# Kernel optimization log

Hardware: AMD Instinct MI355X
Metric: run time of the kernel (lower is better)

## Reference

```python
import jax, jax.numpy as jnp
import numpy as np

N_EMB = 4096
EMB_DIM = 256
BETA = 0.25


def setup_inputs() -> dict:
    key = jax.random.key(0)
    k1, k2 = jax.random.split(key)
    z = jax.random.normal(k1, (32, EMB_DIM, 32, 32), dtype=jnp.float32)
    # nn.Embedding weight initialized uniform(-1/n_emb, 1/n_emb)
    embedding = jax.random.uniform(
        k2, (N_EMB, EMB_DIM), dtype=jnp.float32,
        minval=-1.0 / N_EMB, maxval=1.0 / N_EMB)
    return {"z": z, "embedding": embedding}


def reference(z, embedding):
    sg = jax.lax.stop_gradient
    # (B,C,H,W) -> (B,H,W,C)
    zp = jnp.transpose(z, (0, 2, 3, 1))
    zf = zp.reshape(-1, EMB_DIM)  # [N, D]
    # squared distances: ||z||^2 + ||e||^2 - 2 z e^T  -> [N, n_emb]
    d = (jnp.sum(zf * zf, axis=1, keepdims=True)
         + jnp.sum(embedding * embedding, axis=1)
         - 2.0 * jnp.matmul(zf, embedding.T))
    idx = jnp.argmin(d, axis=1)  # [N]
    min_encodings = jax.nn.one_hot(idx, N_EMB, dtype=zf.dtype)  # [N, n_emb]
    e_mean = jnp.mean(min_encodings, axis=0)
    perplexity = jnp.exp(-jnp.sum(e_mean * jnp.log(e_mean + 1e-10)))
    # gather codebook rows (same math as one-hot matmul)
    z_q = jnp.take(embedding, idx, axis=0).reshape(zp.shape)
    # straight-through estimator
    z_q_st = zp + sg(z_q - zp)
    q_latent_loss = jnp.mean((z_q_st - sg(zp)) ** 2)
    e_latent_loss = jnp.mean((sg(z_q_st) - zp) ** 2)
    loss = q_latent_loss + BETA * e_latent_loss
    z_q_out = jnp.transpose(z_q_st, (0, 3, 1, 2))  # (B,C,H,W)
    return (loss, z_q_out, perplexity, min_encodings, idx[:, None])
```

## Files before the change

### kernel.cpp

```cpp
#include <hip/hip_runtime.h>

#define N_ROWS 32768
#define NEMB   4096
#define DIM    256

#define O_LOSS 0
#define O_ZQ   1ull
#define O_PERP 8388609ull
#define O_ENC  8388610ull
#define O_IDX  142606338ull
#define Z4_BEG 2097153
#define Z4_END 35651584

#define CAP    32
#define EPS    1e-3f

typedef unsigned long long u64;
typedef __attribute__((ext_vector_type(8))) __bf16 bf16x8;
typedef __attribute__((ext_vector_type(4))) float  f32x4;


__device__ __forceinline__ unsigned int f2bf1(float x) {
    unsigned int u = __float_as_uint(x);
    return (u + 0x7fffu + ((u >> 16) & 1u)) >> 16;
}
__device__ __forceinline__ unsigned int f2bf2(float lo, float hi) {
    return f2bf1(lo) | (f2bf1(hi) << 16);
}

__global__ __launch_bounds__(256)
void vq_zero(float* __restrict__ out)
{
    const f32x4 zz = {0.f, 0.f, 0.f, 0.f};
    const size_t base = (size_t)Z4_BEG + (size_t)blockIdx.x * 256 + threadIdx.x;
#pragma unroll
    for (int i = 0; i < 64; ++i) {
        const size_t idx = base + (size_t)i * 524288;
        if (idx < (size_t)Z4_END)
            __builtin_nontemporal_store(zz, (f32x4*)out + idx);
    }
}

__global__ __launch_bounds__(256)
void vq_prep(const float* __restrict__ z, const float* __restrict__ emb,
             unsigned short* __restrict__ zbf, unsigned short* __restrict__ embsw,
             int* __restrict__ counts, float* __restrict__ out)
{
    const int tid = threadIdx.x, blk = blockIdx.x;
    if (blk < 1024) {
        __shared__ float L[32][256];
        const int b = blk >> 5, sub = blk & 31;
        const int c0 = (sub >> 2) << 5;
        const int hw0 = (sub & 3) << 8;
        const float* zp = z + (size_t)b * 262144 + hw0 + tid;
#pragma unroll 8
        for (int i = 0; i < 32; ++i)
            L[i][tid] = zp[(size_t)(c0 + i) << 10];
        __syncthreads();
        const int n = (b << 10) + hw0 + tid;
        unsigned int pk[16];
#pragma unroll
        for (int c2 = 0; c2 < 16; ++c2)
            pk[c2] = f2bf2(L[2 * c2][tid], L[2 * c2 + 1][tid]);
        uint4* dst = (uint4*)((char*)zbf + (size_t)n * 512 + (size_t)c0 * 2);
#pragma unroll
        for (int q = 0; q < 4; ++q)
            dst[q] = make_uint4(pk[4*q], pk[4*q+1], pk[4*q+2], pk[4*q+3]);
    } else {
        const int base = ((blk - 1024) << 8) + tid;
#pragma unroll
        for (int q = 0; q < 4; ++q) {
            const int ch = (base << 2) + q;
            const int code = ch >> 5, cw = ch & 31;
            const float* ep = emb + (size_t)code * 256 + cw * 8;
            float4 e0 = *(const float4*)ep;
            float4 e1 = *(const float4*)(ep + 4);
            uint4 pk = make_uint4(f2bf2(e0.x, e0.y), f2bf2(e0.z, e0.w),
                                  f2bf2(e1.x, e1.y), f2bf2(e1.z, e1.w));
            *(uint4*)((char*)embsw + (size_t)code * 512 + (size_t)((cw ^ (code & 7)) << 4)) = pk;
        }
        if (blk == 1024) {
            for (int j = tid; j < NEMB; j += 256) counts[j] = 0;
            if (tid == 0) {
                out[O_ENC] = 0.f; out[O_ENC + 1] = 0.f;
                out[(size_t)Z4_END * 4] = 0.f; out[(size_t)Z4_END * 4 + 1] = 0.f;
            }
        }
    }
}

__global__ __launch_bounds__(512, 2)
void vq_filter(const float* __restrict__ z, const float* __restrict__ emb,
               const unsigned short* __restrict__ zbf_us,
               const unsigned short* __restrict__ embsw,
               float* __restrict__ out, u64* __restrict__ ws_best)
{
#pragma clang fp contract(off)
    (void)out;
    __shared__ __align__(16) char Bsh[65536];
    __shared__ float zsumS[256];
    __shared__ float rowmaxS[256];
    __shared__ unsigned short rowlist[256][CAP];
    __shared__ int rowcnt[256];
    __shared__ int nflag;
    __shared__ int flagrows[32];
    __shared__ u64 flagbest[32];

    const int tid = threadIdx.x;
    const int blk = blockIdx.x;
    const int rb  = blk >> 1;
    const int hv  = blk & 1;
    const int n0  = rb << 8;
    const int C0  = hv << 11;
    const int b   = n0 >> 10;
    const int hw0 = n0 & 1023;
    const int w    = tid >> 6;
    const int lane = tid & 63;
    const int r0w  = w << 5;
    const int arow = lane & 15;
    const int akg  = lane >> 4;
    const float* zb = z + (size_t)b * 262144 + hw0;

    if (tid < 32) flagbest[tid] = ~0ull;
    if (tid == 0) nflag = 0;

    if (tid < 256) {
        rowcnt[tid] = 0;
        const float* gz = zb + tid;
        float hs0, hs1;
        {
            float r[8];
#pragma unroll
            for (int j = 0; j < 8; ++j) { float v = gz[(size_t)j << 10]; r[j] = v * v; }
            for (int m = 1; m < 16; ++m)
#pragma unroll
                for (int j = 0; j < 8; ++j) {
                    float v = gz[(size_t)(8 * m + j) << 10];
                    float sq = v * v;
                    r[j] = r[j] + sq;
                }
            hs0 = ((r[0] + r[1]) + (r[2] + r[3])) + ((r[4] + r[5]) + (r[6] + r[7]));
        }
        {
            float r[8];
#pragma unroll
            for (int j = 0; j < 8; ++j) { float v = gz[(size_t)(128 + j) << 10]; r[j] = v * v; }
            for (int m = 1; m < 16; ++m)
#pragma unroll
                for (int j = 0; j < 8; ++j) {
                    float v = gz[(size_t)(128 + 8 * m + j) << 10];
                    float sq = v * v;
                    r[j] = r[j] + sq;
                }
            hs1 = ((r[0] + r[1]) + (r[2] + r[3])) + ((r[4] + r[5]) + (r[6] + r[7]));
        }
        zsumS[tid] = hs0 + hs1;
    }

    bf16x8 A[2][8];
#pragma unroll
    for (int rf = 0; rf < 2; ++rf)
#pragma unroll
        for (int s = 0; s < 8; ++s)
            A[rf][s] = *(const bf16x8*)((const char*)zbf_us
                        + ((size_t)(n0 + r0w + rf * 16 + arow) << 9)
                        + (size_t)((s * 32 + akg * 8) << 1));

    auto stage = [&](int buf, int ct) {
        const char* sb = (const char*)embsw + (((size_t)(C0 + (ct << 6))) << 9)
                         + (w << 10) + (lane << 4);
        char* db = Bsh + buf * 32768 + (w << 10);
#pragma unroll
        for (int it = 0; it < 4; ++it) {
            __builtin_amdgcn_global_load_lds(
                (const __attribute__((address_space(1))) unsigned int*)(sb + it * 8192),
                (__attribute__((address_space(3))) unsigned int*)(db + it * 8192),
                16, 0, 0);
        }
    };

    float vmax[2][4];
#pragma unroll
    for (int rf = 0; rf < 2; ++rf)
#pragma unroll
        for (int j = 0; j < 4; ++j) vmax[rf][j] = -3.4e38f;
    float thr[2][4];

    for (int pass = 0; pass < 2; ++pass) {
        stage(0, 0);
        __syncthreads();
        for (int ct = 0; ct < 32; ++ct) {
            const int buf = ct & 1;
            if (ct < 31) stage(buf ^ 1, ct + 1);

            f32x4 acc[2][4];
            const f32x4 zz = {0.f, 0.f, 0.f, 0.f};
#pragma unroll
            for (int rf = 0; rf < 2; ++rf)
#pragma unroll
                for (int cf = 0; cf < 4; ++cf) acc[rf][cf] = zz;

            const char* bufp = Bsh + buf * 32768;
#pragma unroll
            for (int s = 0; s < 8; ++s) {
#pragma unroll
                for (int cf = 0; cf < 4; ++cf) {
                    const int cl = (cf << 4) + arow;
                    const int off = (cl << 9) + (((s << 6) + (akg << 4)) ^ ((cl & 7) << 4));
                    bf16x8 bb = *(const bf16x8*)(bufp + off);
                    acc[0][cf] = __builtin_amdgcn_mfma_f32_16x16x32_bf16(A[0][s], bb, acc[0][cf], 0, 0, 0);
                    acc[1][cf] = __builtin_amdgcn_mfma_f32_16x16x32_bf16(A[1][s], bb, acc[1][cf], 0, 0, 0);
                }
            }

            if (pass == 0) {
#pragma unroll
                for (int rf = 0; rf < 2; ++rf)
#pragma unroll
                    for (int cf = 0; cf < 4; ++cf)
#pragma unroll
                        for (int j = 0; j < 4; ++j)
                            vmax[rf][j] = fmaxf(vmax[rf][j], acc[rf][cf][j]);
            } else {
#pragma unroll
                for (int rf = 0; rf < 2; ++rf)
#pragma unroll
                    for (int cf = 0; cf < 4; ++cf)
#pragma unroll
                        for (int j = 0; j < 4; ++j) {
                            const float v = acc[rf][cf][j];
                            if (v >= thr[rf][j]) {
                                const int row  = r0w + rf * 16 + akg * 4 + j;
                                const int code = (ct << 6) + (cf << 4) + arow;
                                const int slot = atomicAdd(&rowcnt[row], 1);
                                if (slot < CAP) rowlist[row][slot] = (unsigned short)code;
                                else if (slot == CAP) {
                                    const int fi = atomicAdd(&nflag, 1);
                                    if (fi < 32) flagrows[fi] = row;
                                }
                            }
                        }
            }
            __syncthreads();
        }
        if (pass == 0) {
#pragma unroll
            for (int rf = 0; rf < 2; ++rf)
#pragma unroll
                for (int j = 0; j < 4; ++j) {
                    float v = vmax[rf][j];
                    v = fmaxf(v, __shfl_xor(v, 1));
                    v = fmaxf(v, __shfl_xor(v, 2));
                    v = fmaxf(v, __shfl_xor(v, 4));
                    v = fmaxf(v, __shfl_xor(v, 8));
                    vmax[rf][j] = v;
                }
            if ((lane & 15) == 0) {
#pragma unroll
                for (int rf = 0; rf < 2; ++rf)
#pragma unroll
                    for (int j = 0; j < 4; ++j)
                        rowmaxS[r0w + rf * 16 + akg * 4 + j] = vmax[rf][j];
            }
            __syncthreads();
#pragma unroll
            for (int rf = 0; rf < 2; ++rf)
#pragma unroll
                for (int j = 0; j < 4; ++j)
                    thr[rf][j] = rowmaxS[r0w + rf * 16 + akg * 4 + j] - EPS;
        }
    }
    __syncthreads();

    if (tid < 256) {
        const int cnt = rowcnt[tid];
        if (cnt <= CAP) {
            const float zs = zsumS[tid];
            const float* zrow = zb + tid;
            u64 bestk = ~0ull;
            for (int basec = 0; basec < cnt; basec += 8) {
                int codes[8];
#pragma unroll
                for (int j = 0; j < 8; ++j) {
                    const int jj = basec + j;
                    codes[j] = rowlist[tid][jj < cnt ? jj : basec];
                }
                const float* ep[8];
#pragma unroll
                for (int j = 0; j < 8; ++j) ep[j] = emb + ((size_t)(C0 + codes[j]) << 8);
                float a8[8] = {0.f, 0.f, 0.f, 0.f, 0.f, 0.f, 0.f, 0.f};
#pragma unroll 2
                for (int k4 = 0; k4 < 64; ++k4) {
                    const float zv0 = zrow[(size_t)(4 * k4 + 0) << 10];
                    const float zv1 = zrow[(size_t)(4 * k4 + 1) << 10];
                    const float zv2 = zrow[(size_t)(4 * k4 + 2) << 10];
                    const float zv3 = zrow[(size_t)(4 * k4 + 3) << 10];
                    float4 e4[8];
#pragma unroll
                    for (int j = 0; j < 8; ++j) e4[j] = *(const float4*)(ep[j] + 4 * k4);
#pragma unroll
                    for (int j = 0; j < 8; ++j) {
                        a8[j] = fmaf(zv0, e4[j].x, a8[j]);
                        a8[j] = fmaf(zv1, e4[j].y, a8[j]);
                        a8[j] = fmaf(zv2, e4[j].z, a8[j]);
                        a8[j] = fmaf(zv3, e4[j].w, a8[j]);
                    }
                }
#pragma unroll
                for (int j = 0; j < 8; ++j) {
                    if (basec + j < cnt) {
                        const float d = fmaf(-2.f, a8[j], zs);
                        const u64 key = ((u64)__float_as_uint(d) << 32)
                                      | (unsigned)(C0 + codes[j]);
                        if (key < bestk) bestk = key;
                    }
                }
            }
            ws_best[((size_t)(n0 + tid) << 1) + hv] = bestk;
        }
    }
    __syncthreads();

    const int nf = (nflag > 32) ? 32 : nflag;
    for (int f = 0; f < nf; ++f) {
        const int fr = flagrows[f];
        if (tid < 256) {
            const float zs = zsumS[fr];
            const float* zrow = zb + fr;
            const float* ep0 = emb + ((size_t)(C0 + (tid << 3)) << 8);
            float a8[8] = {0.f, 0.f, 0.f, 0.f, 0.f, 0.f, 0.f, 0.f};
#pragma unroll 2
            for (int k4 = 0; k4 < 64; ++k4) {
                const float zv0 = zrow[(size_t)(4 * k4 + 0) << 10];
                const float zv1 = zrow[(size_t)(4 * k4 + 1) << 10];
                const float zv2 = zrow[(size_t)(4 * k4 + 2) << 10];
                const float zv3 = zrow[(size_t)(4 * k4 + 3) << 10];
#pragma unroll
                for (int j = 0; j < 8; ++j) {
                    const float4 e4 = *(const float4*)(ep0 + (size_t)j * 256 + 4 * k4);
                    a8[j] = fmaf(zv0, e4.x, a8[j]);
                    a8[j] = fmaf(zv1, e4.y, a8[j]);
                    a8[j] = fmaf(zv2, e4.z, a8[j]);
                    a8[j] = fmaf(zv3, e4.w, a8[j]);
                }
            }
            u64 bk = ~0ull;
#pragma unroll
            for (int j = 0; j < 8; ++j) {
                const float d = fmaf(-2.f, a8[j], zs);
                const u64 key = ((u64)__float_as_uint(d) << 32)
                              | (unsigned)(C0 + (tid << 3) + j);
                if (key < bk) bk = key;
            }
            atomicMin(&flagbest[f], bk);
        }
    }
    __syncthreads();
    if (tid < nf) ws_best[((size_t)(n0 + flagrows[tid]) << 1) + hv] = flagbest[tid];
}

__global__ void vq_scatter(const u64* __restrict__ ws_best, float* __restrict__ out,
                           int* __restrict__ counts, int* __restrict__ ws_idx)
{
    int i = blockIdx.x * 256 + threadIdx.x;
    if (i < N_ROWS) {
        u64 m = ws_best[(size_t)i * 2];
        u64 v = ws_best[(size_t)i * 2 + 1];
        if (v < m) m = v;
        int id = (int)(m & 0xffffffffu);
        ws_idx[i] = id;
        out[O_IDX + i] = (float)id;
        out[O_ENC + (size_t)i * 4096 + id] = 1.0f;
        atomicAdd(&counts[id], 1);
    }
}

__global__ __launch_bounds__(256)
void vq_zq(const float* __restrict__ z, const float* __restrict__ emb,
           const int* __restrict__ ws_idx, float* __restrict__ out,
           double* __restrict__ parts)
{
#pragma clang fp contract(off)
    double val = 0.0;
#pragma unroll 1
    for (int j = 0; j < 16; ++j) {
        const size_t gid = (size_t)blockIdx.x * 4096 + j * 256 + threadIdx.x;
        const int b   = (int)(gid >> 18);
        const int rem = (int)(gid & 262143);
        const int c   = rem >> 10;
        const int hw  = rem & 1023;
        const int n   = (b << 10) + hw;

        const float zp = z[gid];
        const float e  = emb[(size_t)ws_idx[n] * 256 + c];
        const float t  = e - zp;
        const float zq = zp + t;
        __builtin_nontemporal_store(zq, &out[O_ZQ + gid]);

        const float diff = zq - zp;
        val += (double)(diff * diff);
    }

    __shared__ double red[256];
    red[threadIdx.x] = val;
    __syncthreads();
    for (int st = 128; st > 0; st >>= 1) {
        if ((int)threadIdx.x < st) red[threadIdx.x] += red[threadIdx.x + st];
        __syncthreads();
    }
    if (threadIdx.x == 0) parts[blockIdx.x] = red[0];
}

__global__ void vq_final(const int* __restrict__ counts,
                         const double* __restrict__ parts, float* __restrict__ out)
{
    __shared__ double red[256];
    const int t = threadIdx.x;

    double loc = 0.0;
    for (int j = t; j < NEMB; j += 256) {
        float em = (float)counts[j] * (1.0f / 32768.0f);
        float lt = em + 1e-10f;
        float lg = logf(lt);
        float pr = em * lg;
        loc += (double)pr;
    }
    red[t] = loc;
    __syncthreads();
    for (int st = 128; st > 0; st >>= 1) {
        if (t < st) red[t] += red[t + st];
        __syncthreads();
    }
    double s = red[0];
    __syncthreads();

    double q = 0.0;
    for (int j = t; j < 2048; j += 256) q += parts[j];
    red[t] = q;
    __syncthreads();
    for (int st = 128; st > 0; st >>= 1) {
        if (t < st) red[t] += red[t + st];
        __syncthreads();
    }
    if (t == 0) {
        out[O_PERP] = expf(-(float)s);
        double qm = red[0] * (1.0 / 8388608.0);
        float  qf = (float)qm;
        out[O_LOSS] = qf + 0.25f * qf;
    }
}

extern "C" void kernel_launch(void* const* d_in, const int* in_sizes, int n_in,
                              void* d_out, int out_size, void* d_ws, size_t ws_size,
                              hipStream_t stream)
{
    const float* z   = (const float*)d_in[0];
    const float* emb = (const float*)d_in[1];
    float* out = (float*)d_out;

    u64*    ws_best = (u64*)d_ws;
    int*    counts  = (int*)((char*)d_ws + 1048576);
    double* parts   = (double*)((char*)d_ws + 1064960);
    int*    ws_idx  = (int*)((char*)d_ws + 1081344);

    unsigned short* zbf   = (unsigned short*)((char*)d_out + 16);
    unsigned short* embsw = (unsigned short*)((char*)d_out + 16 + 16777216);

    vq_zero   <<<2048, 256, 0, stream>>>(out);
    vq_prep   <<<1152, 256, 0, stream>>>(z, emb, zbf, embsw, counts, out);
    vq_filter <<<256,  512, 0, stream>>>(z, emb, zbf, embsw, out, ws_best);
    vq_scatter<<<128,  256, 0, stream>>>(ws_best, out, counts, ws_idx);
    vq_zq     <<<2048, 256, 0, stream>>>(z, emb, ws_idx, out, parts);
    vq_final  <<<1,    256, 0, stream>>>(counts, parts, out);
}
```

Baseline: 1.112 ms.

## Single-pass running-max candidate filter, halve rows per block, stage codebook rows in zq

Measured after the change: 1.707 ms. 1.53x slower.

```diff
diff --git a/kernel.cpp b/kernel.cpp
--- a/kernel.cpp
+++ b/kernel.cpp
@@ -93,15 +93,13 @@
 void vq_filter(const float* __restrict__ z, const float* __restrict__ emb,
                const unsigned short* __restrict__ zbf_us,
                const unsigned short* __restrict__ embsw,
-               float* __restrict__ out, u64* __restrict__ ws_best)
+               u64* __restrict__ ws_best)
 {
 #pragma clang fp contract(off)
-    (void)out;
     __shared__ __align__(16) char Bsh[65536];
-    __shared__ float zsumS[256];
-    __shared__ float rowmaxS[256];
-    __shared__ unsigned short rowlist[256][CAP];
-    __shared__ int rowcnt[256];
+    __shared__ float zsumS[128];
+    __shared__ unsigned short rowlist[128][CAP];
+    __shared__ int rowcnt[128];
     __shared__ int nflag;
     __shared__ int flagrows[32];
     __shared__ u64 flagbest[32];
@@ -110,13 +108,13 @@
     const int blk = blockIdx.x;
     const int rb  = blk >> 1;
     const int hv  = blk & 1;
-    const int n0  = rb << 8;
+    const int n0  = rb << 7;
     const int C0  = hv << 11;
     const int b   = n0 >> 10;
     const int hw0 = n0 & 1023;
     const int w    = tid >> 6;
     const int lane = tid & 63;
-    const int r0w  = w << 5;
+    const int r0w  = w << 4;
     const int arow = lane & 15;
     const int akg  = lane >> 4;
     const float* zb = z + (size_t)b * 262144 + hw0;
@@ -124,7 +122,7 @@
     if (tid < 32) flagbest[tid] = ~0ull;
     if (tid == 0) nflag = 0;
 
-    if (tid < 256) {
+    if (tid < 128) {
         rowcnt[tid] = 0;
         const float* gz = zb + tid;
         float hs0, hs1;
@@ -157,14 +155,12 @@
         zsumS[tid] = hs0 + hs1;
     }
 
-    bf16x8 A[2][8];
-#pragma unroll
-    for (int rf = 0; rf < 2; ++rf)
-#pragma unroll
-        for (int s = 0; s < 8; ++s)
-            A[rf][s] = *(const bf16x8*)((const char*)zbf_us
-                        + ((size_t)(n0 + r0w + rf * 16 + arow) << 9)
-                        + (size_t)((s * 32 + akg * 8) << 1));
+    bf16x8 A[8];
+#pragma unroll
+    for (int s = 0; s < 8; ++s)
+        A[s] = *(const bf16x8*)((const char*)zbf_us
+                    + ((size_t)(n0 + r0w + arow) << 9)
+                    + (size_t)((s * 32 + akg * 8) << 1));
 
     auto stage = [&](int buf, int ct) {
         const char* sb = (const char*)embsw + (((size_t)(C0 + (ct << 6))) << 9)
@@ -179,100 +175,62 @@
         }
     };
 
-    float vmax[2][4];
-#pragma unroll
-    for (int rf = 0; rf < 2; ++rf)
-#pragma unroll
-        for (int j = 0; j < 4; ++j) vmax[rf][j] = -3.4e38f;
-    float thr[2][4];
-
-    for (int pass = 0; pass < 2; ++pass) {
-        stage(0, 0);
+    float runmax[4];
+#pragma unroll
+    for (int j = 0; j < 4; ++j) runmax[j] = -3.4e38f;
+
+    stage(0, 0);
+    __syncthreads();
+
+    for (int ct = 0; ct < 32; ++ct) {
+        const int buf = ct & 1;
+        if (ct < 31) stage(buf ^ 1, ct + 1);
+
+        f32x4 acc[4];
+        const f32x4 zz = {0.f, 0.f, 0.f, 0.f};
+#pragma unroll
+        for (int cf = 0; cf < 4; ++cf) acc[cf] = zz;
+
+        const char* bufp = Bsh + buf * 32768;
+#pragma unroll
+        for (int s = 0; s < 8; ++s) {
+#pragma unroll
+            for (int cf = 0; cf < 4; ++cf) {
+                const int cl = (cf << 4) + arow;
+                const int off = (cl << 9) + (((s << 6) + (akg << 4)) ^ ((cl & 7) << 4));
+                bf16x8 bb = *(const bf16x8*)(bufp + off);
+                acc[cf] = __builtin_amdgcn_mfma_f32_16x16x32_bf16(A[s], bb, acc[cf], 0, 0, 0);
+            }
+        }
+
+#pragma unroll
+        for (int j = 0; j < 4; ++j) {
+            float m = fmaxf(fmaxf(acc[0][j], acc[1][j]), fmaxf(acc[2][j], acc[3][j]));
+            m = fmaxf(m, __shfl_xor(m, 1));
+            m = fmaxf(m, __shfl_xor(m, 2));
+            m = fmaxf(m, __shfl_xor(m, 4));
+            m = fmaxf(m, __shfl_xor(m, 8));
+            const float rm = fmaxf(runmax[j], m);
+            runmax[j] = rm;
+            const float th = rm - EPS;
+#pragma unroll
+            for (int cf = 0; cf < 4; ++cf) {
+                if (acc[cf][j] >= th) {
+                    const int row  = r0w + akg * 4 + j;
+                    const int code = (ct << 6) + (cf << 4) + arow;
+                    const int slot = atomicAdd(&rowcnt[row], 1);
+                    if (slot < CAP) rowlist[row][slot] = (unsigned short)code;
+                    else if (slot == CAP) {
+                        const int fi = atomicAdd(&nflag, 1);
+                        if (fi < 32) flagrows[fi] = row;
+                    }
+                }
+            }
+        }
         __syncthreads();
-        for (int ct = 0; ct < 32; ++ct) {
-            const int buf = ct & 1;
-            if (ct < 31) stage(buf ^ 1, ct + 1);
-
-            f32x4 acc[2][4];
-            const f32x4 zz = {0.f, 0.f, 0.f, 0.f};
-#pragma unroll
-            for (int rf = 0; rf < 2; ++rf)
-#pragma unroll
-                for (int cf = 0; cf < 4; ++cf) acc[rf][cf] = zz;
-
-            const char* bufp = Bsh + buf * 32768;
-#pragma unroll
-            for (int s = 0; s < 8; ++s) {
-#pragma unroll
-                for (int cf = 0; cf < 4; ++cf) {
-                    const int cl = (cf << 4) + arow;
-                    const int off = (cl << 9) + (((s << 6) + (akg << 4)) ^ ((cl & 7) << 4));
-                    bf16x8 bb = *(const bf16x8*)(bufp + off);
-                    acc[0][cf] = __builtin_amdgcn_mfma_f32_16x16x32_bf16(A[0][s], bb, acc[0][cf], 0, 0, 0);
-                    acc[1][cf] = __builtin_amdgcn_mfma_f32_16x16x32_bf16(A[1][s], bb, acc[1][cf], 0, 0, 0);
-                }
-            }
-
-            if (pass == 0) {
-#pragma unroll
-                for (int rf = 0; rf < 2; ++rf)
-#pragma unroll
-                    for (int cf = 0; cf < 4; ++cf)
-#pragma unroll
-                        for (int j = 0; j < 4; ++j)
-                            vmax[rf][j] = fmaxf(vmax[rf][j], acc[rf][cf][j]);
-            } else {
-#pragma unroll
-                for (int rf = 0; rf < 2; ++rf)
-#pragma unroll
-                    for (int cf = 0; cf < 4; ++cf)
-#pragma unroll
-                        for (int j = 0; j < 4; ++j) {
-                            const float v = acc[rf][cf][j];
-                            if (v >= thr[rf][j]) {
-                                const int row  = r0w + rf * 16 + akg * 4 + j;
-                                const int code = (ct << 6) + (cf << 4) + arow;
-                                const int slot = atomicAdd(&rowcnt[row], 1);
-                                if (slot < CAP) rowlist[row][slot] = (unsigned short)code;
-                                else if (slot == CAP) {
-                                    const int fi = atomicAdd(&nflag, 1);
-                                    if (fi < 32) flagrows[fi] = row;
-                                }
-                            }
-                        }
-            }
-            __syncthreads();
-        }
-        if (pass == 0) {
-#pragma unroll
-            for (int rf = 0; rf < 2; ++rf)
-#pragma unroll
-                for (int j = 0; j < 4; ++j) {
-                    float v = vmax[rf][j];
-                    v = fmaxf(v, __shfl_xor(v, 1));
-                    v = fmaxf(v, __shfl_xor(v, 2));
-                    v = fmaxf(v, __shfl_xor(v, 4));
-                    v = fmaxf(v, __shfl_xor(v, 8));
-                    vmax[rf][j] = v;
-                }
-            if ((lane & 15) == 0) {
-#pragma unroll
-                for (int rf = 0; rf < 2; ++rf)
-#pragma unroll
-                    for (int j = 0; j < 4; ++j)
-                        rowmaxS[r0w + rf * 16 + akg * 4 + j] = vmax[rf][j];
-            }
-            __syncthreads();
-#pragma unroll
-            for (int rf = 0; rf < 2; ++rf)
-#pragma unroll
-                for (int j = 0; j < 4; ++j)
-                    thr[rf][j] = rowmaxS[r0w + rf * 16 + akg * 4 + j] - EPS;
-        }
-    }
-    __syncthreads();
-
-    if (tid < 256) {
+    }
+
+    if (tid < 128) {
         const int cnt = rowcnt[tid];
         if (cnt <= CAP) {
             const float zs = zsumS[tid];
@@ -381,34 +339,58 @@
            double* __restrict__ parts)
 {
 #pragma clang fp contract(off)
+    __shared__ float embT[32][257];
+    __shared__ int idxS[32];
+    __shared__ double red[256];
+
+    const int tid = threadIdx.x;
+    const int blk = blockIdx.x;
+    const int b   = blk >> 5;
+    const int hw0 = (blk & 31) << 5;
+    const int n0  = (b << 10) + hw0;
+
+    if (tid < 32) idxS[tid] = ws_idx[n0 + tid];
+    __syncthreads();
+
+    {
+        const int g = tid >> 3, l8 = tid & 7;
+        const float* er = emb + (size_t)idxS[g] * 256;
+#pragma unroll
+        for (int it = 0; it < 8; ++it) {
+            const float4 v = *(const float4*)(er + it * 32 + l8 * 4);
+            const int c = it * 32 + l8 * 4;
+            embT[g][c]     = v.x;
+            embT[g][c + 1] = v.y;
+            embT[g][c + 2] = v.z;
+            embT[g][c + 3] = v.w;
+        }
+    }
+    __syncthreads();
+
+    const int r  = tid & 31;
+    const int cq = tid >> 5;
+    const size_t base = (size_t)b * 262144 + hw0 + r;
     double val = 0.0;
-#pragma unroll 1
-    for (int j = 0; j < 16; ++j) {
-        const size_t gid = (size_t)blockIdx.x * 4096 + j * 256 + threadIdx.x;
-        const int b   = (int)(gid >> 18);
-        const int rem = (int)(gid & 262143);
-        const int c   = rem >> 10;
-        const int hw  = rem & 1023;
-        const int n   = (b << 10) + hw;
-
+#pragma unroll 4
+    for (int i = 0; i < 32; ++i) {
+        const int c = i * 8 + cq;
+        const size_t gid = base + (size_t)c * 1024;
         const float zp = z[gid];
-        const float e  = emb[(size_t)ws_idx[n] * 256 + c];
+        const float e  = embT[r][c];
         const float t  = e - zp;
         const float zq = zp + t;
         __builtin_nontemporal_store(zq, &out[O_ZQ + gid]);
-
         const float diff = zq - zp;
         val += (double)(diff * diff);
     }
 
-    __shared__ double red[256];
-    red[threadIdx.x] = val;
+    red[tid] = val;
     __syncthreads();
     for (int st = 128; st > 0; st >>= 1) {
-        if ((int)threadIdx.x < st) red[threadIdx.x] += red[threadIdx.x + st];
+        if (tid < st) red[tid] += red[tid + st];
         __syncthreads();
     }
-    if (threadIdx.x == 0) parts[blockIdx.x] = red[0];
+    if (tid == 0) parts[blk] = red[0];
 }
 
 __global__ void vq_final(const int* __restrict__ counts,
@@ -435,7 +417,7 @@
     __syncthreads();
 
     double q = 0.0;
-    for (int j = t; j < 2048; j += 256) q += parts[j];
+    for (int j = t; j < 1024; j += 256) q += parts[j];
     red[t] = q;
     __syncthreads();
     for (int st = 128; st > 0; st >>= 1) {
@@ -468,8 +450,8 @@
 
     vq_zero   <<<2048, 256, 0, stream>>>(out);
     vq_prep   <<<1152, 256, 0, stream>>>(z, emb, zbf, embsw, counts, out);
-    vq_filter <<<256,  512, 0, stream>>>(z, emb, zbf, embsw, out, ws_best);
+    vq_filter <<<512,  512, 0, stream>>>(z, emb, zbf, embsw, ws_best);
     vq_scatter<<<128,  256, 0, stream>>>(ws_best, out, counts, ws_idx);
-    vq_zq     <<<2048, 256, 0, stream>>>(z, emb, ws_idx, out, parts);
+    vq_zq     <<<1024, 256, 0, stream>>>(z, emb, ws_idx, out, parts);
     vq_final  <<<1,    256, 0, stream>>>(counts, parts, out);
 }
```
